# Optimization experiments

Measured on AMD Instinct MI355X. Metric: run time of the kernel, lower is better.

Reference implementation:

```python
import jax, jax.numpy as jnp
import numpy as np

N = 50000      # nodes
E = 800000     # edges
D_IN = 128     # input_dim
D = 128        # hidden_dim
H = 8          # num_heads
DH = D // H    # head dim
S = 10         # security_feature_dim
LN_EPS = 1e-5


def setup_inputs() -> dict:
    key = jax.random.key(0)
    ks = jax.random.split(key, 16)
    def lin_w(k, fin, fout):
        return (jax.random.normal(k, (fin, fout), jnp.float32) / np.sqrt(fin)).astype(jnp.float32)
    return {
        "x": jax.random.normal(ks[0], (N, D_IN), jnp.float32),
        "edge_index": jax.random.randint(ks[1], (2, E), 0, N, jnp.int64),
        "security_features": jax.random.normal(ks[2], (N, S), jnp.float32),
        "W1": lin_w(ks[3], D_IN, D), "b1": jnp.zeros((D,), jnp.float32),
        "W2": lin_w(ks[4], D, D),    "b2": jnp.zeros((D,), jnp.float32),
        "Wq": lin_w(ks[5], D, D),    "bq": jnp.zeros((D,), jnp.float32),
        "Wk": lin_w(ks[6], D, D),    "bk": jnp.zeros((D,), jnp.float32),
        "Wv": lin_w(ks[7], D, D),    "bv": jnp.zeros((D,), jnp.float32),
        "Wsec": lin_w(ks[8], S, H),  "bsec": jnp.zeros((H,), jnp.float32),
        "Wo": lin_w(ks[9], D, D),    "bo": jnp.zeros((D,), jnp.float32),
        "ln1_g": jnp.ones((D,), jnp.float32), "ln1_b": jnp.zeros((D,), jnp.float32),
        "ln2_g": jnp.ones((D,), jnp.float32), "ln2_b": jnp.zeros((D,), jnp.float32),
    }


def _layer_norm(x, g, b):
    m = jnp.mean(x, axis=-1, keepdims=True)
    v = jnp.mean(jnp.square(x - m), axis=-1, keepdims=True)
    return (x - m) * jax.lax.rsqrt(v + LN_EPS) * g + b


def reference(x, edge_index, security_features,
              W1, b1, W2, b2, Wq, bq, Wk, bk, Wv, bv,
              Wsec, bsec, Wo, bo, ln1_g, ln1_b, ln2_g, ln2_b):
    # h = relu(linear1(x))  -- [N, D]
    h = jax.nn.relu(x @ W1 + b1)

    # SecurityAwareAttention: edge-wise multi-head attention with a
    # per-edge security bias derived from the source node's security features.
    q = (h @ Wq + bq).reshape(N, H, DH)
    k = (h @ Wk + bk).reshape(N, H, DH)
    v = (h @ Wv + bv).reshape(N, H, DH)
    src, dst = edge_index[0], edge_index[1]

    sec_bias = security_features @ Wsec + bsec            # [N, H]
    scores = jnp.einsum('ehd,ehd->eh', q[dst], k[src]) / np.sqrt(DH) + sec_bias[src]  # [E, H]

    # segment softmax over incoming edges of each destination node
    m = jax.ops.segment_max(scores, dst, num_segments=N)  # [N, H]
    e = jnp.exp(scores - m[dst])
    s = jax.ops.segment_sum(e, dst, num_segments=N)       # [N, H]
    attn = e / (s[dst] + 1e-9)                            # [E, H]

    agg = jax.ops.segment_sum(attn[:, :, None] * v[src], dst, num_segments=N)  # [N, H, DH]
    attended = agg.reshape(N, D) @ Wo + bo

    # dropout is identity (eval mode)
    out = _layer_norm(h + attended, ln1_g, ln1_b)
    out = _layer_norm(out + jax.nn.relu(out @ W2 + b2), ln2_g, ln2_b)
    return (out, attn)
```

## Files before the change

kernel.cpp:

```cpp
#include <hip/hip_runtime.h>
#include <hip/hip_bf16.h>
#include <math.h>

#define N_NODES 50000
#define N_EDGES 800000
#define DIM 128
#define NHEAD 8
#define DHEAD 16
#define SDIM 10
#define NSCAN_BLK 196
#define SETUP_W 48
#define SETUP_CNT 3125
#define SETUP_SEC 1563

typedef __attribute__((ext_vector_type(8))) short bf16x8;
typedef __attribute__((ext_vector_type(4))) float f32x4;

__device__ __forceinline__ float bf2f(unsigned short u) {
    return __uint_as_float(((unsigned)u) << 16);
}
__device__ __forceinline__ unsigned short f2bf(float f) {
    unsigned u = __float_as_uint(f);
    return (unsigned short)((u + 0x7FFFu + ((u >> 16) & 1u)) >> 16);
}

__global__ __launch_bounds__(256) void setup_kernel(
    const float* __restrict__ W1, const float* __restrict__ Wq,
    const float* __restrict__ Wk, const float* __restrict__ Wv,
    const float* __restrict__ Wo, const float* __restrict__ W2,
    unsigned short* __restrict__ Wt, const int* __restrict__ dst,
    int* __restrict__ deg, const float* __restrict__ sec,
    const float* __restrict__ Wsec, const float* __restrict__ bsec,
    float* __restrict__ secb) {
    const int b = blockIdx.x, t = threadIdx.x;
    if (b < SETUP_W) {
        const int mtx = b >> 3, slice = b & 7;
        const float* W = (mtx == 0) ? W1 : (mtx == 1) ? Wq : (mtx == 2) ? Wk :
                         (mtx == 3) ? Wv : (mtx == 4) ? Wo : W2;
        unsigned short* o = Wt + mtx * 16384;
#pragma unroll
        for (int i = 0; i < 8; ++i) {
            int idx = slice * 2048 + t + 256 * i;
            int k = idx >> 7, n = idx & 127;
            o[n * 128 + k] = f2bf(W[idx]);
        }
    } else if (b < SETUP_W + SETUP_CNT) {
        int e = (b - SETUP_W) * 256 + t;
        if (e < N_EDGES) atomicAdd(&deg[dst[e]], 1);
    } else {
        int idx = (b - SETUP_W - SETUP_CNT) * 256 + t;
        if (idx < N_NODES * NHEAD) {
            int n = idx >> 3, h = idx & 7;
            float acc = bsec[h];
#pragma unroll
            for (int j = 0; j < SDIM; ++j)
                acc = fmaf(sec[n * SDIM + j], Wsec[j * NHEAD + h], acc);
            secb[idx] = acc;
        }
    }
}

__global__ __launch_bounds__(256) void blocksum_kernel(const int* __restrict__ deg,
                                                       int* __restrict__ bsum) {
    const int t = threadIdx.x;
    int idx = blockIdx.x * 256 + t;
    int v = (idx < N_NODES) ? deg[idx] : 0;
#pragma unroll
    for (int m = 32; m; m >>= 1) v += __shfl_xor(v, m);
    __shared__ int ws[4];
    if ((t & 63) == 0) ws[t >> 6] = v;
    __syncthreads();
    if (t == 0) bsum[blockIdx.x] = ws[0] + ws[1] + ws[2] + ws[3];
}

__global__ __launch_bounds__(256) void scanfin2_kernel(const int* __restrict__ deg,
                                                       const int* __restrict__ bsum,
                                                       int* __restrict__ rowstart) {
    const int t = threadIdx.x, b = blockIdx.x;
    int v0 = (t < b) ? bsum[t] : 0;
#pragma unroll
    for (int m = 32; m; m >>= 1) v0 += __shfl_xor(v0, m);
    __shared__ int ws[4];
    if ((t & 63) == 0) ws[t >> 6] = v0;
    __syncthreads();
    const int bexc = ws[0] + ws[1] + ws[2] + ws[3];

    int idx = b * 256 + t;
    int v = (idx < N_NODES) ? deg[idx] : 0;
    __shared__ int s[256];
    __syncthreads();
    s[t] = v;
    __syncthreads();
#pragma unroll
    for (int off = 1; off < 256; off <<= 1) {
        int x = (t >= off) ? s[t - off] : 0;
        __syncthreads();
        s[t] += x;
        __syncthreads();
    }
    if (idx < N_NODES) rowstart[idx] = bexc + s[t] - v;
    if (b == 0 && t == 0) rowstart[N_NODES] = N_EDGES;
}

__global__ __launch_bounds__(256) void fill_csr_kernel(
    const int* __restrict__ src, const int* __restrict__ dst,
    const int* __restrict__ rowstart, int* __restrict__ ctr,
    int2* __restrict__ epair) {
    int e = blockIdx.x * 256 + threadIdx.x;
    if (e >= N_EDGES) return;
    int d = dst[e];
    int pos = atomicAdd(&ctr[d], 1);
    epair[rowstart[d] + pos] = make_int2(src[e], e);
}

__global__ __launch_bounds__(512) void gemm_hqkv_kernel(
    const float* __restrict__ X, const unsigned short* __restrict__ Wt,
    const float* __restrict__ b1, const float* __restrict__ bq,
    const float* __restrict__ bk, const float* __restrict__ bv,
    unsigned short* __restrict__ hb, unsigned short* __restrict__ qo,
    unsigned short* __restrict__ ko, unsigned short* __restrict__ vo, int nrows) {
    __shared__ alignas(16) unsigned char Wl[32768];
    __shared__ alignas(16) unsigned char Ht[32768];
    const int t = threadIdx.x;
    const int l = t & 63, wave = t >> 6;
    const int l15 = l & 15, lg = l >> 4;
    const int r0 = blockIdx.x * 128 + wave * 16;
    const int arow = r0 + l15;
    const bool aok = arow < nrows;
    const int orow0 = r0 + lg * 4;
    unsigned char* HtW = Ht + wave * 4096;

#pragma unroll
    for (int i = 0; i < 4; ++i) {
        int c = t + 512 * i;
        int n = c >> 4, s = c & 15;
        bf16x8 val = *(const bf16x8*)(Wt + c * 8);
        *(bf16x8*)(Wl + n * 256 + ((s * 16) ^ ((n & 7) << 4))) = val;
    }
    bf16x8 af[4];
#pragma unroll
    for (int k0 = 0; k0 < 4; ++k0) {
        float4 a0 = {0.f, 0.f, 0.f, 0.f}, a1 = {0.f, 0.f, 0.f, 0.f};
        if (aok) {
            const float4* ap = (const float4*)(X + (size_t)arow * DIM + k0 * 32 + lg * 8);
            a0 = ap[0]; a1 = ap[1];
        }
        bf16x8 f;
        f[0] = (short)f2bf(a0.x); f[1] = (short)f2bf(a0.y);
        f[2] = (short)f2bf(a0.z); f[3] = (short)f2bf(a0.w);
        f[4] = (short)f2bf(a1.x); f[5] = (short)f2bf(a1.y);
        f[6] = (short)f2bf(a1.z); f[7] = (short)f2bf(a1.w);
        af[k0] = f;
    }
    __syncthreads();

    {
        f32x4 acc[8];
#pragma unroll
        for (int n = 0; n < 8; ++n) acc[n] = (f32x4){0.f, 0.f, 0.f, 0.f};
#pragma unroll
        for (int k0 = 0; k0 < 4; ++k0) {
#pragma unroll
            for (int n = 0; n < 8; ++n) {
                int row = n * 16 + l15;
                int kb = (k0 * 64 + lg * 16) ^ ((row & 7) << 4);
                bf16x8 bfr = *(bf16x8*)(Wl + row * 256 + kb);
                acc[n] = __builtin_amdgcn_mfma_f32_16x16x32_bf16(af[k0], bfr, acc[n], 0, 0, 0);
            }
        }
#pragma unroll
        for (int n = 0; n < 8; ++n) {
            int col = n * 16 + l15;
            float bvv = b1[col];
#pragma unroll
            for (int i = 0; i < 4; ++i) {
                int rloc = lg * 4 + i;
                unsigned short hv = f2bf(fmaxf(acc[n][i] + bvv, 0.f));
                if (orow0 + i < nrows) hb[(size_t)(orow0 + i) * DIM + col] = hv;
                *(unsigned short*)(HtW + ((rloc * 256 + col * 2) ^ ((rloc & 7) << 4))) = hv;
            }
        }
    }
    __syncthreads();

    bf16x8 af2[4];
#pragma unroll
    for (int k0 = 0; k0 < 4; ++k0)
        af2[k0] = *(const bf16x8*)(HtW + ((l15 * 256 + k0 * 64 + lg * 16) ^ ((l15 & 7) << 4)));

    for (int m = 0; m < 3; ++m) {
        const unsigned short* wsrc = (m == 0) ? Wt + 16384 : (m == 1) ? Wt + 32768 : Wt + 49152;
        const float* bias = (m == 0) ? bq : (m == 1) ? bk : bv;
        unsigned short* outp = (m == 0) ? qo : (m == 1) ? ko : vo;
#pragma unroll
        for (int i = 0; i < 4; ++i) {
            int c = t + 512 * i;
            int n = c >> 4, s = c & 15;
            bf16x8 val = *(const bf16x8*)(wsrc + c * 8);
            *(bf16x8*)(Wl + n * 256 + ((s * 16) ^ ((n & 7) << 4))) = val;
        }
        __syncthreads();
        f32x4 acc[8];
#pragma unroll
        for (int n = 0; n < 8; ++n) acc[n] = (f32x4){0.f, 0.f, 0.f, 0.f};
#pragma unroll
        for (int k0 = 0; k0 < 4; ++k0) {
#pragma unroll
            for (int n = 0; n < 8; ++n) {
                int row = n * 16 + l15;
                int kb = (k0 * 64 + lg * 16) ^ ((row & 7) << 4);
                bf16x8 bfr = *(bf16x8*)(Wl + row * 256 + kb);
                acc[n] = __builtin_amdgcn_mfma_f32_16x16x32_bf16(af2[k0], bfr, acc[n], 0, 0, 0);
            }
        }
#pragma unroll
        for (int n = 0; n < 8; ++n) {
            int col = n * 16 + l15;
            float bvv = bias[col];
#pragma unroll
            for (int i = 0; i < 4; ++i) {
                int r = orow0 + i;
                if (r < nrows) outp[(size_t)r * DIM + col] = f2bf(acc[n][i] + bvv);
            }
        }
        __syncthreads();
    }
}

__global__ __launch_bounds__(256) void node_attn_kernel(
    const unsigned short* __restrict__ qb, const unsigned short* __restrict__ kb,
    const unsigned short* __restrict__ vb, const float* __restrict__ secb,
    const int2* __restrict__ epair, const int* __restrict__ rowstart,
    float* __restrict__ attn_out, unsigned short* __restrict__ aggb) {
    int node = blockIdx.x * 4 + (threadIdx.x >> 6);
    if (node >= N_NODES) return;
    const int lane = threadIdx.x & 63;
    const int start = rowstart[node];
    const int deg = rowstart[node + 1] - start;
    if (deg == 0) {
        ((unsigned*)(aggb + (size_t)node * DIM))[lane] = 0u;
        return;
    }
    const int h = lane & 7;
    const int le = lane >> 3;
    const int hc = le;

    float qv[16];
    {
        const bf16x8* qp = (const bf16x8*)(qb + (size_t)node * DIM + h * DHEAD);
        bf16x8 q0 = qp[0], q1 = qp[1];
#pragma unroll
        for (int i = 0; i < 8; ++i) {
            qv[i] = bf2f((unsigned short)q0[i]);
            qv[8 + i] = bf2f((unsigned short)q1[i]);
        }
    }

    if (deg <= 64) {
        int sall = 0, eall = 0;
        if (lane < deg) {
            int2 p = epair[start + lane];
            sall = p.x;
            eall = p.y;
        }
        float sc[8];
        float m = -INFINITY;
#pragma unroll
        for (int t = 0; t < 8; ++t) {
            sc[t] = -INFINITY;
            if (t * 8 < deg) {
                int jj = t * 8 + le;
                bool valid = jj < deg;
                int s = __shfl(sall, valid ? jj : deg - 1);
                const bf16x8* kp = (const bf16x8*)(kb + (size_t)s * DIM + h * DHEAD);
                bf16x8 k0 = kp[0], k1 = kp[1];
                float acc = 0.f;
#pragma unroll
                for (int i = 0; i < 8; ++i) {
                    acc = fmaf(qv[i], bf2f((unsigned short)k0[i]), acc);
                    acc = fmaf(qv[8 + i], bf2f((unsigned short)k1[i]), acc);
                }
                if (valid) sc[t] = acc * 0.25f + secb[s * NHEAD + h];
            }
            m = fmaxf(m, sc[t]);
        }
        m = fmaxf(m, __shfl_xor(m, 8));
        m = fmaxf(m, __shfl_xor(m, 16));
        m = fmaxf(m, __shfl_xor(m, 32));

        float ev[8];
        float ssum = 0.f;
#pragma unroll
        for (int t = 0; t < 8; ++t) {
            ev[t] = (t * 8 + le < deg) ? __expf(sc[t] - m) : 0.f;
            ssum += ev[t];
        }
        ssum += __shfl_xor(ssum, 8);
        ssum += __shfl_xor(ssum, 16);
        ssum += __shfl_xor(ssum, 32);
        const float rinv = 1.f / (ssum + 1e-9f);

        float2 acc2 = {0.f, 0.f};
#pragma unroll
        for (int t = 0; t < 8; ++t) {
            if (t * 8 < deg) {
#pragma unroll
                for (int le2 = 0; le2 < 8; ++le2) {
                    int jj = t * 8 + le2;
                    int s = __shfl(sall, (jj < deg) ? jj : deg - 1);
                    float evd = __shfl(ev[t], le2 * 8 + hc);
                    unsigned vv = ((const unsigned*)(vb + (size_t)s * DIM))[lane];
                    acc2.x = fmaf(evd, bf2f((unsigned short)(vv & 0xFFFFu)), acc2.x);
                    acc2.y = fmaf(evd, bf2f((unsigned short)(vv >> 16)), acc2.y);
                }
            }
        }
        const float rinv_c = __shfl(rinv, hc);
        unsigned short o0 = f2bf(acc2.x * rinv_c);
        unsigned short o1 = f2bf(acc2.y * rinv_c);
        ((unsigned*)(aggb + (size_t)node * DIM))[lane] =
            (unsigned)o0 | ((unsigned)o1 << 16);

#pragma unroll
        for (int t = 0; t < 8; ++t) {
            int jj = t * 8 + le;
            int e = __shfl(eall, (jj < deg) ? jj : 0);
            if (jj < deg) attn_out[(size_t)e * NHEAD + h] = ev[t] * rinv;
        }
        return;
    }

    float m = -INFINITY;
    for (int j = 0; j < deg; j += 8) {
        int jj = j + le;
        float sc = -INFINITY;
        if (jj < deg) {
            int2 p = epair[start + jj];
            int s = p.x;
            const bf16x8* kp = (const bf16x8*)(kb + (size_t)s * DIM + h * DHEAD);
            bf16x8 k0 = kp[0], k1 = kp[1];
            float acc = 0.f;
#pragma unroll
            for (int i = 0; i < 8; ++i) {
                acc = fmaf(qv[i], bf2f((unsigned short)k0[i]), acc);
                acc = fmaf(qv[8 + i], bf2f((unsigned short)k1[i]), acc);
            }
            sc = acc * 0.25f + secb[s * NHEAD + h];
            attn_out[(size_t)p.y * NHEAD + h] = sc;
        }
        m = fmaxf(m, sc);
    }
    m = fmaxf(m, __shfl_xor(m, 8));
    m = fmaxf(m, __shfl_xor(m, 16));
    m = fmaxf(m, __shfl_xor(m, 32));

    float ssum = 0.f;
    float2 acc2 = {0.f, 0.f};
    for (int j = 0; j < deg; j += 8) {
        int jj = j + le;
        float ev = 0.f;
        if (jj < deg) {
            int e = epair[start + jj].y;
            ev = __expf(attn_out[(size_t)e * NHEAD + h] - m);
        }
        ssum += ev;
        int lim = deg - j; if (lim > 8) lim = 8;
        for (int le2 = 0; le2 < lim; ++le2) {
            float evd = __shfl(ev, le2 * 8 + hc);
            int s = epair[start + j + le2].x;
            unsigned vv = ((const unsigned*)(vb + (size_t)s * DIM))[lane];
            acc2.x = fmaf(evd, bf2f((unsigned short)(vv & 0xFFFFu)), acc2.x);
            acc2.y = fmaf(evd, bf2f((unsigned short)(vv >> 16)), acc2.y);
        }
    }
    ssum += __shfl_xor(ssum, 8);
    ssum += __shfl_xor(ssum, 16);
    ssum += __shfl_xor(ssum, 32);
    const float rinv = 1.f / (ssum + 1e-9f);
    const float rinv_c = __shfl(rinv, hc);

    unsigned short o0 = f2bf(acc2.x * rinv_c);
    unsigned short o1 = f2bf(acc2.y * rinv_c);
    ((unsigned*)(aggb + (size_t)node * DIM))[lane] =
        (unsigned)o0 | ((unsigned)o1 << 16);

    for (int j = 0; j < deg; j += 8) {
        int jj = j + le;
        if (jj < deg) {
            int e = epair[start + jj].y;
            float sc = attn_out[(size_t)e * NHEAD + h];
            attn_out[(size_t)e * NHEAD + h] = __expf(sc - m) * rinv;
        }
    }
}

__global__ __launch_bounds__(512) void gemm_ln12_kernel(
    const unsigned short* __restrict__ A,
    const unsigned short* __restrict__ Wt,
    const float* __restrict__ bo, const float* __restrict__ b2,
    const unsigned short* __restrict__ resid,
    const float* __restrict__ g1, const float* __restrict__ be1,
    const float* __restrict__ g2, const float* __restrict__ be2,
    float* __restrict__ outp, int nrows) {
    __shared__ alignas(16) unsigned char Wl[32768];
    __shared__ alignas(16) unsigned char Mt[32768];
    const int t = threadIdx.x;
    const int l = t & 63, wave = t >> 6;
    const int l15 = l & 15, lg = l >> 4;
    const int r0 = blockIdx.x * 128 + wave * 16;
    const int arow = r0 + l15;
    const bool aok = arow < nrows;
    const int orow0 = r0 + lg * 4;
    unsigned char* MtW = Mt + wave * 4096;

#pragma unroll
    for (int i = 0; i < 4; ++i) {
        int c = t + 512 * i;
        int n = c >> 4, s = c & 15;
        bf16x8 val = *(const bf16x8*)(Wt + c * 8);
        *(bf16x8*)(Wl + n * 256 + ((s * 16) ^ ((n & 7) << 4))) = val;
    }
    bf16x8 af[4];
#pragma unroll
    for (int k0 = 0; k0 < 4; ++k0) {
        bf16x8 z = (bf16x8){0, 0, 0, 0, 0, 0, 0, 0};
        af[k0] = aok ? *(const bf16x8*)(A + (size_t)arow * DIM + k0 * 32 + lg * 8) : z;
    }
    __syncthreads();

    float mid[8][4];
    {
        f32x4 acc[8];
#pragma unroll
        for (int n = 0; n < 8; ++n) acc[n] = (f32x4){0.f, 0.f, 0.f, 0.f};
#pragma unroll
        for (int k0 = 0; k0 < 4; ++k0) {
#pragma unroll
            for (int n = 0; n < 8; ++n) {
                int row = n * 16 + l15;
                int kb = (k0 * 64 + lg * 16) ^ ((row & 7) << 4);
                bf16x8 bfr = *(bf16x8*)(Wl + row * 256 + kb);
                acc[n] = __builtin_amdgcn_mfma_f32_16x16x32_bf16(af[k0], bfr, acc[n], 0, 0, 0);
            }
        }
        float bv[8], gv[8], bev[8];
#pragma unroll
        for (int n = 0; n < 8; ++n) {
            int col = n * 16 + l15;
            bv[n] = bo[col]; gv[n] = g1[col]; bev[n] = be1[col];
        }
#pragma unroll
        for (int i = 0; i < 4; ++i) {
            int r = orow0 + i;
            int rloc = lg * 4 + i;
            float xv[8];
            float s = 0.f;
            if (r < nrows) {
#pragma unroll
                for (int n = 0; n < 8; ++n) {
                    float val = acc[n][i] + bv[n]
                              + bf2f(resid[(size_t)r * DIM + n * 16 + l15]);
                    xv[n] = val;
                    s += val;
                }
            } else {
#pragma unroll
                for (int n = 0; n < 8; ++n) xv[n] = 0.f;
            }
            s += __shfl_xor(s, 1); s += __shfl_xor(s, 2);
            s += __shfl_xor(s, 4); s += __shfl_xor(s, 8);
            float mean = s * (1.f / 128.f);
            float var = 0.f;
#pragma unroll
            for (int n = 0; n < 8; ++n) {
                float d = xv[n] - mean;
                var += d * d;
            }
            var += __shfl_xor(var, 1); var += __shfl_xor(var, 2);
            var += __shfl_xor(var, 4); var += __shfl_xor(var, 8);
            float rstd = rsqrtf(var * (1.f / 128.f) + 1e-5f);
#pragma unroll
            for (int n = 0; n < 8; ++n) {
                int col = n * 16 + l15;
                unsigned short mb = f2bf((xv[n] - mean) * rstd * gv[n] + bev[n]);
                mid[n][i] = bf2f(mb);
                *(unsigned short*)(MtW + ((rloc * 256 + col * 2) ^ ((rloc & 7) << 4))) = mb;
            }
        }
    }
    __syncthreads();

    bf16x8 af2[4];
#pragma unroll
    for (int k0 = 0; k0 < 4; ++k0)
        af2[k0] = *(const bf16x8*)(MtW + ((l15 * 256 + k0 * 64 + lg * 16) ^ ((l15 & 7) << 4)));

#pragma unroll
    for (int i = 0; i < 4; ++i) {
        int c = t + 512 * i;
        int n = c >> 4, s = c & 15;
        bf16x8 val = *(const bf16x8*)(Wt + 16384 + c * 8);
        *(bf16x8*)(Wl + n * 256 + ((s * 16) ^ ((n & 7) << 4))) = val;
    }
    __syncthreads();

    {
        f32x4 acc[8];
#pragma unroll
        for (int n = 0; n < 8; ++n) acc[n] = (f32x4){0.f, 0.f, 0.f, 0.f};
#pragma unroll
        for (int k0 = 0; k0 < 4; ++k0) {
#pragma unroll
            for (int n = 0; n < 8; ++n) {
                int row = n * 16 + l15;
                int kb = (k0 * 64 + lg * 16) ^ ((row & 7) << 4);
                bf16x8 bfr = *(bf16x8*)(Wl + row * 256 + kb);
                acc[n] = __builtin_amdgcn_mfma_f32_16x16x32_bf16(af2[k0], bfr, acc[n], 0, 0, 0);
            }
        }
        float bv[8], gv[8], bev[8];
#pragma unroll
        for (int n = 0; n < 8; ++n) {
            int col = n * 16 + l15;
            bv[n] = b2[col]; gv[n] = g2[col]; bev[n] = be2[col];
        }
#pragma unroll
        for (int i = 0; i < 4; ++i) {
            int r = orow0 + i;
            float xv[8];
            float s = 0.f;
#pragma unroll
            for (int n = 0; n < 8; ++n) {
                float val = fmaxf(acc[n][i] + bv[n], 0.f) + mid[n][i];
                xv[n] = val;
                s += val;
            }
            s += __shfl_xor(s, 1); s += __shfl_xor(s, 2);
            s += __shfl_xor(s, 4); s += __shfl_xor(s, 8);
            float mean = s * (1.f / 128.f);
            float var = 0.f;
#pragma unroll
            for (int n = 0; n < 8; ++n) {
                float d = xv[n] - mean;
                var += d * d;
            }
            var += __shfl_xor(var, 1); var += __shfl_xor(var, 2);
            var += __shfl_xor(var, 4); var += __shfl_xor(var, 8);
            float rstd = rsqrtf(var * (1.f / 128.f) + 1e-5f);
            if (r < nrows) {
#pragma unroll
                for (int n = 0; n < 8; ++n) {
                    int col = n * 16 + l15;
                    outp[(size_t)r * DIM + col] = (xv[n] - mean) * rstd * gv[n] + bev[n];
                }
            }
        }
    }
}

extern "C" void kernel_launch(void* const* d_in, const int* in_sizes, int n_in,
                              void* d_out, int out_size, void* d_ws, size_t ws_size,
                              hipStream_t stream) {
    const float* x    = (const float*)d_in[0];
    const int*   ei   = (const int*)d_in[1];
    const float* sec  = (const float*)d_in[2];
    const float* W1   = (const float*)d_in[3];
    const float* b1   = (const float*)d_in[4];
    const float* W2   = (const float*)d_in[5];
    const float* b2   = (const float*)d_in[6];
    const float* Wq   = (const float*)d_in[7];
    const float* bq   = (const float*)d_in[8];
    const float* Wk   = (const float*)d_in[9];
    const float* bk   = (const float*)d_in[10];
    const float* Wv   = (const float*)d_in[11];
    const float* bvp  = (const float*)d_in[12];
    const float* Wsec = (const float*)d_in[13];
    const float* bsec = (const float*)d_in[14];
    const float* Wo   = (const float*)d_in[15];
    const float* bo   = (const float*)d_in[16];
    const float* g1   = (const float*)d_in[17];
    const float* be1  = (const float*)d_in[18];
    const float* g2   = (const float*)d_in[19];
    const float* be2  = (const float*)d_in[20];

    const int* srcp = ei;
    const int* dstp = ei + N_EDGES;

    char* wsb = (char*)d_ws;
    unsigned short* hb   = (unsigned short*)(wsb);
    unsigned short* qbu  = (unsigned short*)(wsb + 12800000);
    unsigned short* kbu  = (unsigned short*)(wsb + 25600000);
    unsigned short* vbu  = (unsigned short*)(wsb + 38400000);
    unsigned short* aggb = (unsigned short*)(wsb + 51200000);
    float* secb          = (float*)(wsb + 76800000);
    unsigned short* Wt   = (unsigned short*)(wsb + 78400000);
    int* deg             = (int*)(wsb + 78600000);
    int* ctr             = (int*)(wsb + 78800000);
    int* rowstart        = (int*)(wsb + 79000000);
    int2* epair          = (int2*)(wsb + 79200256);
    int* bsum            = (int*)(wsb + 85600512);

    float* outp = (float*)d_out;
    float* attn = outp + (size_t)N_NODES * DIM;

    dim3 blk(256);
    const int big_grid = (N_NODES + 127) / 128;
    const int egrid = (N_EDGES + 255) / 256;
    const int wgrid = (N_NODES + 3) / 4;

    hipMemsetAsync(deg, 0, 400000, stream);

    setup_kernel<<<SETUP_W + SETUP_CNT + SETUP_SEC, blk, 0, stream>>>(
        W1, Wq, Wk, Wv, Wo, W2, Wt, dstp, deg, sec, Wsec, bsec, secb);
    blocksum_kernel<<<NSCAN_BLK, blk, 0, stream>>>(deg, bsum);
    scanfin2_kernel<<<NSCAN_BLK, blk, 0, stream>>>(deg, bsum, rowstart);
    fill_csr_kernel<<<egrid, blk, 0, stream>>>(srcp, dstp, rowstart, ctr, epair);

    gemm_hqkv_kernel<<<big_grid, dim3(512), 0, stream>>>(x, Wt, b1, bq, bk, bvp,
                                                         hb, qbu, kbu, vbu, N_NODES);

    node_attn_kernel<<<wgrid, blk, 0, stream>>>(qbu, kbu, vbu, secb, epair,
                                                rowstart, attn, aggb);

    gemm_ln12_kernel<<<big_grid, dim3(512), 0, stream>>>(aggb, Wt + 65536, bo, b2, hb,
                                                         g1, be1, g2, be2, outp, N_NODES);
}
```

Measured before the change: 216.6 us.

## Fuse CSR fill into QKV GEMM launch and use fp16 dot2 for scores

Merges the CSR fill kernel into the h/q/k/v GEMM launch as extra blocks, so edge scattering and the projection GEMM run concurrently in one launch. Q and K are now stored as fp16 instead of bf16, and attention scores use packed fdot2 instructions, which cuts per-edge conversion and FMA work. The extra blocks reserve the GEMM's shared memory even though they don't use it, which may limit occupancy. fp16 storage changes precision and range compared with bf16.

```diff
diff --git a/kernel.cpp b/kernel.cpp
--- a/kernel.cpp
+++ b/kernel.cpp
@@ -1,5 +1,6 @@
 #include <hip/hip_runtime.h>
 #include <hip/hip_bf16.h>
+#include <hip/hip_fp16.h>
 #include <math.h>
 
 #define N_NODES 50000
@@ -12,9 +13,18 @@
 #define SETUP_W 48
 #define SETUP_CNT 3125
 #define SETUP_SEC 1563
+#define HQKV_GRID 391
+#define FILL_GRID 1563
 
 typedef __attribute__((ext_vector_type(8))) short bf16x8;
 typedef __attribute__((ext_vector_type(4))) float f32x4;
+typedef _Float16 h16x2 __attribute__((ext_vector_type(2)));
+
+#if __has_builtin(__builtin_amdgcn_fdot2)
+#define HAVE_FDOT2 1
+#else
+#define HAVE_FDOT2 0
+#endif
 
 __device__ __forceinline__ float bf2f(unsigned short u) {
     return __uint_as_float(((unsigned)u) << 16);
@@ -23,6 +33,16 @@
     unsigned u = __float_as_uint(f);
     return (unsigned short)((u + 0x7FFFu + ((u >> 16) & 1u)) >> 16);
 }
+__device__ __forceinline__ unsigned short f2h(float f) {
+    __half h = __float2half(f);
+    return *reinterpret_cast<unsigned short*>(&h);
+}
+__device__ __forceinline__ float h2f(unsigned short u) {
+    __half h = *reinterpret_cast<__half*>(&u);
+    return __half2float(h);
+}
+
+union frag16 { bf16x8 v[2]; h16x2 h[8]; unsigned short u[16]; };
 
 __global__ __launch_bounds__(256) void setup_kernel(
     const float* __restrict__ W1, const float* __restrict__ Wq,
@@ -102,18 +122,10 @@
     if (b == 0 && t == 0) rowstart[N_NODES] = N_EDGES;
 }
 
-__global__ __launch_bounds__(256) void fill_csr_kernel(
+__global__ __launch_bounds__(512) void fill_hqkv_kernel(
     const int* __restrict__ src, const int* __restrict__ dst,
     const int* __restrict__ rowstart, int* __restrict__ ctr,
-    int2* __restrict__ epair) {
-    int e = blockIdx.x * 256 + threadIdx.x;
-    if (e >= N_EDGES) return;
-    int d = dst[e];
-    int pos = atomicAdd(&ctr[d], 1);
-    epair[rowstart[d] + pos] = make_int2(src[e], e);
-}
-
-__global__ __launch_bounds__(512) void gemm_hqkv_kernel(
+    int2* __restrict__ epair,
     const float* __restrict__ X, const unsigned short* __restrict__ Wt,
     const float* __restrict__ b1, const float* __restrict__ bq,
     const float* __restrict__ bk, const float* __restrict__ bv,
@@ -122,6 +134,17 @@
     __shared__ alignas(16) unsigned char Wl[32768];
     __shared__ alignas(16) unsigned char Ht[32768];
     const int t = threadIdx.x;
+
+    if (blockIdx.x >= HQKV_GRID) {
+        int e = (blockIdx.x - HQKV_GRID) * 512 + t;
+        if (e < N_EDGES) {
+            int d = dst[e];
+            int pos = atomicAdd(&ctr[d], 1);
+            epair[rowstart[d] + pos] = make_int2(src[e], e);
+        }
+        return;
+    }
+
     const int l = t & 63, wave = t >> 6;
     const int l15 = l & 15, lg = l >> 4;
     const int r0 = blockIdx.x * 128 + wave * 16;
@@ -220,11 +243,31 @@
 #pragma unroll
             for (int i = 0; i < 4; ++i) {
                 int r = orow0 + i;
-                if (r < nrows) outp[(size_t)r * DIM + col] = f2bf(acc[n][i] + bvv);
+                if (r < nrows) {
+                    float val = acc[n][i] + bvv;
+                    outp[(size_t)r * DIM + col] = (m < 2) ? f2h(val) : f2bf(val);
+                }
             }
         }
         __syncthreads();
     }
+}
+
+__device__ __forceinline__ float score_dot(const frag16& q, const frag16& k) {
+#if HAVE_FDOT2
+    float a0 = 0.f, a1 = 0.f;
+#pragma unroll
+    for (int i = 0; i < 4; ++i) {
+        a0 = __builtin_amdgcn_fdot2(q.h[2 * i], k.h[2 * i], a0, false);
+        a1 = __builtin_amdgcn_fdot2(q.h[2 * i + 1], k.h[2 * i + 1], a1, false);
+    }
+    return a0 + a1;
+#else
+    float acc = 0.f;
+#pragma unroll
+    for (int i = 0; i < 16; ++i) acc = fmaf(h2f(q.u[i]), h2f(k.u[i]), acc);
+    return acc;
+#endif
 }
 
 __global__ __launch_bounds__(256) void node_attn_kernel(
@@ -245,15 +288,10 @@
     const int le = lane >> 3;
     const int hc = le;
 
-    float qv[16];
+    frag16 qf;
     {
         const bf16x8* qp = (const bf16x8*)(qb + (size_t)node * DIM + h * DHEAD);
-        bf16x8 q0 = qp[0], q1 = qp[1];
-#pragma unroll
-        for (int i = 0; i < 8; ++i) {
-            qv[i] = bf2f((unsigned short)q0[i]);
-            qv[8 + i] = bf2f((unsigned short)q1[i]);
-        }
+        qf.v[0] = qp[0]; qf.v[1] = qp[1];
     }
 
     if (deg <= 64) {
@@ -273,13 +311,9 @@
                 bool valid = jj < deg;
                 int s = __shfl(sall, valid ? jj : deg - 1);
                 const bf16x8* kp = (const bf16x8*)(kb + (size_t)s * DIM + h * DHEAD);
-                bf16x8 k0 = kp[0], k1 = kp[1];
-                float acc = 0.f;
-#pragma unroll
-                for (int i = 0; i < 8; ++i) {
-                    acc = fmaf(qv[i], bf2f((unsigned short)k0[i]), acc);
-                    acc = fmaf(qv[8 + i], bf2f((unsigned short)k1[i]), acc);
-                }
+                frag16 kf;
+                kf.v[0] = kp[0]; kf.v[1] = kp[1];
+                float acc = score_dot(qf, kf);
                 if (valid) sc[t] = acc * 0.25f + secb[s * NHEAD + h];
             }
             m = fmaxf(m, sc[t]);
@@ -338,13 +372,9 @@
             int2 p = epair[start + jj];
             int s = p.x;
             const bf16x8* kp = (const bf16x8*)(kb + (size_t)s * DIM + h * DHEAD);
-            bf16x8 k0 = kp[0], k1 = kp[1];
-            float acc = 0.f;
-#pragma unroll
-            for (int i = 0; i < 8; ++i) {
-                acc = fmaf(qv[i], bf2f((unsigned short)k0[i]), acc);
-                acc = fmaf(qv[8 + i], bf2f((unsigned short)k1[i]), acc);
-            }
+            frag16 kf;
+            kf.v[0] = kp[0]; kf.v[1] = kp[1];
+            float acc = score_dot(qf, kf);
             sc = acc * 0.25f + secb[s * NHEAD + h];
             attn_out[(size_t)p.y * NHEAD + h] = sc;
         }
@@ -604,8 +634,6 @@
     float* attn = outp + (size_t)N_NODES * DIM;
 
     dim3 blk(256);
-    const int big_grid = (N_NODES + 127) / 128;
-    const int egrid = (N_EDGES + 255) / 256;
     const int wgrid = (N_NODES + 3) / 4;
 
     hipMemsetAsync(deg, 0, 400000, stream);
@@ -614,14 +642,14 @@
         W1, Wq, Wk, Wv, Wo, W2, Wt, dstp, deg, sec, Wsec, bsec, secb);
     blocksum_kernel<<<NSCAN_BLK, blk, 0, stream>>>(deg, bsum);
     scanfin2_kernel<<<NSCAN_BLK, blk, 0, stream>>>(deg, bsum, rowstart);
-    fill_csr_kernel<<<egrid, blk, 0, stream>>>(srcp, dstp, rowstart, ctr, epair);
-
-    gemm_hqkv_kernel<<<big_grid, dim3(512), 0, stream>>>(x, Wt, b1, bq, bk, bvp,
-                                                         hb, qbu, kbu, vbu, N_NODES);
+
+    fill_hqkv_kernel<<<HQKV_GRID + FILL_GRID, dim3(512), 0, stream>>>(
+        srcp, dstp, rowstart, ctr, epair,
+        x, Wt, b1, bq, bk, bvp, hb, qbu, kbu, vbu, N_NODES);
 
     node_attn_kernel<<<wgrid, blk, 0, stream>>>(qbu, kbu, vbu, secb, epair,
                                                 rowstart, attn, aggb);
 
-    gemm_ln12_kernel<<<big_grid, dim3(512), 0, stream>>>(aggb, Wt + 65536, bo, b2, hb,
-                                                         g1, be1, g2, be2, outp, N_NODES);
-}
+    gemm_ln12_kernel<<<HQKV_GRID, dim3(512), 0, stream>>>(aggb, Wt + 65536, bo, b2, hb,
+                                                          g1, be1, g2, be2, outp, N_NODES);
+}
```

Result: faster. 194.9 us (-10.1%).
